# Kernel tuning notes

Measured on AMD Instinct MI355X. Metric: run time of the kernel, lower is better.

Reference implementation:

```python
import jax, jax.numpy as jnp
import numpy as np

N = 50000
E = 800000
IN_C = 128
HID = 64
OUT_C = 64
NUM_CLASSES = 10
H1 = 2
H2 = 1
NEG_SLOPE = 0.2  # PyG GATv2Conv default


def setup_inputs() -> dict:
    key = jax.random.key(0)
    ks = jax.random.split(key, 12)
    s = 0.05
    inp = {
        "x": jax.random.normal(ks[0], (N, IN_C), jnp.float32),
        "edge_index": jax.random.randint(ks[1], (2, E), 0, N, jnp.int64),
        "batch": jnp.zeros((N,), jnp.int64),
        # conv1 params (GATv2: separate lin_l / lin_r, att vector, output bias)
        "Wl1": jax.random.normal(ks[2], (H1 * HID, IN_C), jnp.float32) * s,
        "bl1": jnp.zeros((H1 * HID,), jnp.float32),
        "Wr1": jax.random.normal(ks[3], (H1 * HID, IN_C), jnp.float32) * s,
        "br1": jnp.zeros((H1 * HID,), jnp.float32),
        "att1": jax.random.normal(ks[4], (H1, HID), jnp.float32) * s,
        "bias1": jnp.zeros((H1 * HID,), jnp.float32),
        # conv2 params
        "Wl2": jax.random.normal(ks[5], (H2 * OUT_C, H1 * HID), jnp.float32) * s,
        "bl2": jnp.zeros((H2 * OUT_C,), jnp.float32),
        "Wr2": jax.random.normal(ks[6], (H2 * OUT_C, H1 * HID), jnp.float32) * s,
        "br2": jnp.zeros((H2 * OUT_C,), jnp.float32),
        "att2": jax.random.normal(ks[7], (H2, OUT_C), jnp.float32) * s,
        "bias2": jnp.zeros((OUT_C,), jnp.float32),
        # classifier head
        "Wc": jax.random.normal(ks[8], (NUM_CLASSES, OUT_C), jnp.float32) * s,
        "bc": jnp.zeros((NUM_CLASSES,), jnp.float32),
    }
    return inp


def _gatv2_conv(x, src, dst, Wl, bl, Wr, br, att, bias, heads, ch, concat):
    n = x.shape[0]
    xl = (x @ Wl.T + bl).reshape(n, heads, ch)  # messages from source
    xr = (x @ Wr.T + br).reshape(n, heads, ch)  # target-side transform
    e = xl[src] + xr[dst]                        # [Etot, H, C]
    e = jnp.where(e > 0, e, NEG_SLOPE * e)       # LeakyReLU
    score = jnp.einsum('ehc,hc->eh', e, att)     # [Etot, H]
    # segment softmax over incoming edges of each dst node
    m = jax.ops.segment_max(score, dst, num_segments=n)  # [N, H]
    m = jnp.where(jnp.isfinite(m), m, 0.0)
    ex = jnp.exp(score - m[dst])
    denom = jax.ops.segment_sum(ex, dst, num_segments=n)  # [N, H]
    alpha = ex / denom[dst]
    out = jax.ops.segment_sum(alpha[:, :, None] * xl[src], dst, num_segments=n)  # [N,H,C]
    if concat:
        out = out.reshape(n, heads * ch)
    else:
        out = out.mean(axis=1)
    return out + bias


def reference(x, edge_index, batch, Wl1, bl1, Wr1, br1, att1, bias1,
              Wl2, bl2, Wr2, br2, att2, bias2, Wc, bc):
    n = x.shape[0]
    # PyG GATv2Conv adds self-loops by default
    loops = jnp.arange(n, dtype=edge_index.dtype)
    src = jnp.concatenate([edge_index[0], loops])
    dst = jnp.concatenate([edge_index[1], loops])

    h = _gatv2_conv(x, src, dst, Wl1, bl1, Wr1, br1, att1, bias1, H1, HID, True)
    h = jax.nn.elu(h)  # dropout p=0 / eval -> identity
    h = _gatv2_conv(h, src, dst, Wl2, bl2, Wr2, br2, att2, bias2, H2, OUT_C, False)
    h = jax.nn.elu(h)
    logits = h @ Wc.T + bc  # [N, num_classes]
    return logits
```

## Files before the change

kernel.cpp:

```cpp
#include <hip/hip_runtime.h>
#include <hip/hip_bf16.h>

#define N_NODES 50000
#define E_EDGES 800000
#define NCLS 10
#define SCAN_BLOCKS 196

typedef short bfrag __attribute__((ext_vector_type(8)));
typedef float f32x4 __attribute__((ext_vector_type(4)));

__device__ __forceinline__ int rfl(int v) { return __builtin_amdgcn_readfirstlane(v); }

__device__ __forceinline__ unsigned short bf16rne(float x) {
    unsigned u = __float_as_uint(x);
    unsigned r = u + 0x7FFFu + ((u >> 16) & 1u);
    return (unsigned short)(r >> 16);
}

template <int CTRL, int RM>
__device__ __forceinline__ float dppadd(float x) {
    int s = __builtin_amdgcn_update_dpp(0, __float_as_int(x), CTRL, RM, 0xf, true);
    return x + __int_as_float(s);
}
__device__ __forceinline__ float rl63(float x) {
    return __int_as_float(__builtin_amdgcn_readlane(__float_as_int(x), 63));
}
__device__ __forceinline__ float rl31(float x) {
    return __int_as_float(__builtin_amdgcn_readlane(__float_as_int(x), 31));
}
__device__ __forceinline__ void dred1(float& x0) {
    x0 = dppadd<0x111, 0xf>(x0);
    x0 = dppadd<0x112, 0xf>(x0);
    x0 = dppadd<0x114, 0xf>(x0);
    x0 = dppadd<0x118, 0xf>(x0);
    x0 = dppadd<0x142, 0xa>(x0);
    x0 = dppadd<0x143, 0xc>(x0);
}
__device__ __forceinline__ void dred4(float& x0, float& x1, float& x2, float& x3) {
    x0 = dppadd<0x111, 0xf>(x0); x1 = dppadd<0x111, 0xf>(x1);
    x2 = dppadd<0x111, 0xf>(x2); x3 = dppadd<0x111, 0xf>(x3);
    x0 = dppadd<0x112, 0xf>(x0); x1 = dppadd<0x112, 0xf>(x1);
    x2 = dppadd<0x112, 0xf>(x2); x3 = dppadd<0x112, 0xf>(x3);
    x0 = dppadd<0x114, 0xf>(x0); x1 = dppadd<0x114, 0xf>(x1);
    x2 = dppadd<0x114, 0xf>(x2); x3 = dppadd<0x114, 0xf>(x3);
    x0 = dppadd<0x118, 0xf>(x0); x1 = dppadd<0x118, 0xf>(x1);
    x2 = dppadd<0x118, 0xf>(x2); x3 = dppadd<0x118, 0xf>(x3);
    x0 = dppadd<0x142, 0xa>(x0); x1 = dppadd<0x142, 0xa>(x1);
    x2 = dppadd<0x142, 0xa>(x2); x3 = dppadd<0x142, 0xa>(x3);
    x0 = dppadd<0x143, 0xc>(x0); x1 = dppadd<0x143, 0xc>(x1);
    x2 = dppadd<0x143, 0xc>(x2); x3 = dppadd<0x143, 0xc>(x3);
}
__device__ __forceinline__ void dredH(float& x) {
    x = dppadd<0x111, 0xf>(x);
    x = dppadd<0x112, 0xf>(x);
    x = dppadd<0x114, 0xf>(x);
    x = dppadd<0x118, 0xf>(x);
    x = dppadd<0x142, 0xa>(x);
}
__device__ __forceinline__ void dredH2(float& x, float& y) {
    x = dppadd<0x111, 0xf>(x); y = dppadd<0x111, 0xf>(y);
    x = dppadd<0x112, 0xf>(x); y = dppadd<0x112, 0xf>(y);
    x = dppadd<0x114, 0xf>(x); y = dppadd<0x114, 0xf>(y);
    x = dppadd<0x118, 0xf>(x); y = dppadd<0x118, 0xf>(y);
    x = dppadd<0x142, 0xa>(x); y = dppadd<0x142, 0xa>(y);
}
__device__ __forceinline__ float lrelu(float u) { return u > 0.f ? u : 0.2f * u; }
__device__ __forceinline__ float escore(float2 v, float2 xr2, float2 av) {
    float ux = v.x + xr2.x, uy = v.y + xr2.y;
    ux = fmaxf(ux, 0.2f * ux);
    uy = fmaxf(uy, 0.2f * uy);
    return ux * av.x + uy * av.y;
}

__global__ void k_count(const int* __restrict__ dst, int* __restrict__ deg) {
    int i = blockIdx.x * blockDim.x + threadIdx.x;
    if (i < E_EDGES) {
        unsigned d = (unsigned)dst[i];
        if (d < N_NODES) atomicAdd(&deg[d], 1);
    }
}

__global__ void k_scanA(const int* __restrict__ deg, int* __restrict__ incl,
                        int* __restrict__ bsum) {
    __shared__ int s[256];
    int i = blockIdx.x * 256 + threadIdx.x;
    int v = (i < N_NODES) ? deg[i] : 0;
    s[threadIdx.x] = v;
    __syncthreads();
    for (int off = 1; off < 256; off <<= 1) {
        int t = (threadIdx.x >= off) ? s[threadIdx.x - off] : 0;
        __syncthreads();
        s[threadIdx.x] += t;
        __syncthreads();
    }
    if (i < N_NODES) incl[i] = s[threadIdx.x];
    if (threadIdx.x == 255) bsum[blockIdx.x] = s[255];
}

__global__ void k_scanB(int* __restrict__ bsum) {
    __shared__ int s[256];
    int t = threadIdx.x;
    s[t] = (t < SCAN_BLOCKS) ? bsum[t] : 0;
    __syncthreads();
    for (int off = 1; off < 256; off <<= 1) {
        int v = (t >= off) ? s[t - off] : 0;
        __syncthreads();
        s[t] += v;
        __syncthreads();
    }
    if (t < SCAN_BLOCKS) bsum[t] = s[t];
}

__global__ void k_scanC(int* __restrict__ degcur, const int* __restrict__ incl,
                        const int* __restrict__ bsum, int* __restrict__ rowptr) {
    int i = blockIdx.x * 256 + threadIdx.x;
    if (i >= N_NODES) return;
    int base = (blockIdx.x == 0) ? 0 : bsum[blockIdx.x - 1];
    int d = degcur[i];
    int excl = base + incl[i] - d;
    rowptr[i] = excl;
    degcur[i] = excl;
    if (i == N_NODES - 1) rowptr[N_NODES] = base + incl[i];
}

__global__ void k_scatter(const int* __restrict__ src, const int* __restrict__ dst,
                          int* __restrict__ cursor, int* __restrict__ csr_src) {
    int i = blockIdx.x * blockDim.x + threadIdx.x;
    if (i < E_EDGES) {
        unsigned d = (unsigned)dst[i];
        if (d < N_NODES) {
            int p = atomicAdd(&cursor[d], 1);
            unsigned s = (unsigned)src[i];
            csr_src[p] = (s < N_NODES) ? (int)s : 0;
        }
    }
}

__global__ void k_splitW2(const float* __restrict__ WL, const float* __restrict__ WR,
                          int n, short* __restrict__ hiL, short* __restrict__ loL,
                          short* __restrict__ hiR, short* __restrict__ loR) {
    int i = blockIdx.x * 256 + threadIdx.x;
    if (i < n) {
        float x = WL[i];
        unsigned short h = bf16rne(x);
        float hf = __uint_as_float((unsigned)h << 16);
        hiL[i] = (short)h;
        loL[i] = (short)bf16rne(x - hf);
        float y = WR[i];
        unsigned short h2 = bf16rne(y);
        float hf2 = __uint_as_float((unsigned)h2 << 16);
        hiR[i] = (short)h2;
        loR[i] = (short)bf16rne(y - hf2);
    }
}

template <int NOUT>
__global__ __launch_bounds__(256) void k_mgemmS(const float* __restrict__ X,
                                                const short* __restrict__ whiL,
                                                const short* __restrict__ wloL,
                                                const short* __restrict__ whiR,
                                                const short* __restrict__ wloR,
                                                const float* __restrict__ bL,
                                                const float* __restrict__ bR,
                                                float* __restrict__ YL,
                                                float* __restrict__ YR, int nrows) {
    const int NCT = 4;
    const short* whi = blockIdx.z ? whiR : whiL;
    const short* wlo = blockIdx.z ? wloR : wloL;
    const float* b   = blockIdx.z ? bR : bL;
    float* Y         = blockIdx.z ? YR : YL;
    int tid = threadIdx.x;
    int wv = tid >> 6, lane = tid & 63;
    int m = lane & 15, g = lane >> 4;
    int colbase = blockIdx.y * 64;
    int row = blockIdx.x * 64 + wv * 16 + m;
    int rowc = min(row, nrows - 1);

    bfrag ahi[4], alo[4];
    const float* xp = X + (size_t)rowc * 128 + g * 8;
#pragma unroll
    for (int kb = 0; kb < 4; ++kb) {
        float4 u0 = *(const float4*)(xp + kb * 32);
        float4 u1 = *(const float4*)(xp + kb * 32 + 4);
        float xs[8] = {u0.x, u0.y, u0.z, u0.w, u1.x, u1.y, u1.z, u1.w};
#pragma unroll
        for (int j = 0; j < 8; ++j) {
            unsigned short h = bf16rne(xs[j]);
            float hf = __uint_as_float((unsigned)h << 16);
            unsigned short l = bf16rne(xs[j] - hf);
            ahi[kb][j] = (short)h;
            alo[kb][j] = (short)l;
        }
    }

    f32x4 acc[NCT];
#pragma unroll
    for (int ct = 0; ct < NCT; ++ct) acc[ct] = (f32x4){0.f, 0.f, 0.f, 0.f};

#pragma unroll
    for (int kb = 0; kb < 4; ++kb) {
#pragma unroll
        for (int ct = 0; ct < NCT; ++ct) {
            size_t wo = (size_t)(colbase + ct * 16 + m) * 128 + kb * 32 + g * 8;
            bfrag bh = *(const bfrag*)(whi + wo);
            bfrag bl_ = *(const bfrag*)(wlo + wo);
            acc[ct] = __builtin_amdgcn_mfma_f32_16x16x32_bf16(ahi[kb], bh, acc[ct], 0, 0, 0);
            acc[ct] = __builtin_amdgcn_mfma_f32_16x16x32_bf16(alo[kb], bh, acc[ct], 0, 0, 0);
            acc[ct] = __builtin_amdgcn_mfma_f32_16x16x32_bf16(ahi[kb], bl_, acc[ct], 0, 0, 0);
        }
    }

    int orow0 = blockIdx.x * 64 + wv * 16 + g * 4;
#pragma unroll
    for (int ct = 0; ct < NCT; ++ct) {
        int col = colbase + ct * 16 + m;
        float bv = b[col];
#pragma unroll
        for (int i = 0; i < 4; ++i) {
            int orow = orow0 + i;
            if (orow < nrows) Y[(size_t)orow * NOUT + col] = acc[ct][i] + bv;
        }
    }
}

__global__ __launch_bounds__(256) void k_gat1(const float* __restrict__ xl,
                                              const float* __restrict__ xr,
                                              const int* __restrict__ rowptr,
                                              const int* __restrict__ csr,
                                              const float* __restrict__ att,
                                              const float* __restrict__ bias,
                                              float* __restrict__ out) {
    int node = blockIdx.x * 4 + (threadIdx.x >> 6);
    if (node >= N_NODES) return;
    node = rfl(node);
    int lane = threadIdx.x & 63;
    bool lo = lane < 32;
    const float2* xl2 = (const float2*)xl;
    size_t nb = (size_t)node * 64;
    float2 av = ((const float2*)att)[lane];
    float2 xr2 = ((const float2*)xr)[nb + lane];
    float2 sl2 = xl2[nb + lane];

    float p = escore(sl2, xr2, av);
    dredH(p);
    float sv = lo ? rl31(p) : rl63(p);
    float ev = __expf(sv);
    float den = ev;
    float2 acc;
    acc.x = ev * sl2.x;
    acc.y = ev * sl2.y;

    int beg = rfl(rowptr[node]), end = rfl(rowptr[node + 1]);
    int cnt = end - beg;
    int np = cnt >> 1;
    if (np > 0) {
        const int* cp = csr + beg;
        int i0 = rfl(cp[0]), i1 = rfl(cp[1]);
        float2 A = xl2[(size_t)(unsigned)i0 * 64 + lane];
        float2 B = xl2[(size_t)(unsigned)i1 * 64 + lane];
        for (int q = 1; q <= np; ++q) {
            float2 nA = {0.f, 0.f}, nB = {0.f, 0.f};
            if (q < np) {
                int j0 = rfl(cp[2 * q]), j1 = rfl(cp[2 * q + 1]);
                nA = xl2[(size_t)(unsigned)j0 * 64 + lane];
                nB = xl2[(size_t)(unsigned)j1 * 64 + lane];
            }
            float pa = escore(A, xr2, av);
            float pb = escore(B, xr2, av);
            dredH2(pa, pb);
            float sa = lo ? rl31(pa) : rl63(pa);
            float sb = lo ? rl31(pb) : rl63(pb);
            float eva = __expf(sa);
            float evb = __expf(sb);
            den += eva + evb;
            acc.x = fmaf(eva, A.x, fmaf(evb, B.x, acc.x));
            acc.y = fmaf(eva, A.y, fmaf(evb, B.y, acc.y));
            A = nA; B = nB;
        }
    }
    if (cnt & 1) {
        int j = rfl(csr[end - 1]);
        float2 C = xl2[(size_t)(unsigned)j * 64 + lane];
        float pc = escore(C, xr2, av);
        dredH(pc);
        float sc = lo ? rl31(pc) : rl63(pc);
        float evc = __expf(sc);
        den += evc;
        acc.x = fmaf(evc, C.x, acc.x);
        acc.y = fmaf(evc, C.y, acc.y);
    }
    float2 b2 = ((const float2*)bias)[lane];
    float ox = acc.x / den + b2.x;
    float oy = acc.y / den + b2.y;
    ox = ox > 0.f ? ox : expm1f(ox);
    oy = oy > 0.f ? oy : expm1f(oy);
    float2 o2 = {ox, oy};
    ((float2*)out)[nb + lane] = o2;
}

__global__ __launch_bounds__(256) void k_gat2(const float* __restrict__ xl,
                                              const float* __restrict__ xr,
                                              const int* __restrict__ rowptr,
                                              const int* __restrict__ csr,
                                              const float* __restrict__ att,
                                              const float* __restrict__ bias,
                                              float* __restrict__ out) {
    int node = blockIdx.x * 4 + (threadIdx.x >> 6);
    if (node >= N_NODES) return;
    node = rfl(node);
    int lane = threadIdx.x & 63;
    float a = att[lane];
    size_t nb = (size_t)node << 6;
    float xrv = xr[nb + lane];
    float slv = xl[nb + lane];
    float p = lrelu(slv + xrv) * a;
    dred1(p);
    float w = __expf(rl63(p));
    float den = w;
    float acc = w * slv;

    int beg = rfl(rowptr[node]), end = rfl(rowptr[node + 1]);
    int cnt = end - beg;
    int quads = cnt >> 2;
    if (quads > 0) {
        const int* cp = csr + beg;
        int i0 = rfl(cp[0]), i1 = rfl(cp[1]), i2 = rfl(cp[2]), i3 = rfl(cp[3]);
        float A = (xl + ((size_t)(unsigned)i0 << 6))[lane];
        float B = (xl + ((size_t)(unsigned)i1 << 6))[lane];
        float C = (xl + ((size_t)(unsigned)i2 << 6))[lane];
        float D = (xl + ((size_t)(unsigned)i3 << 6))[lane];
        for (int q = 1; q <= quads; ++q) {
            float nA = 0.f, nB = 0.f, nC = 0.f, nD = 0.f;
            if (q < quads) {
                int j0 = rfl(cp[4 * q]), j1 = rfl(cp[4 * q + 1]);
                int j2 = rfl(cp[4 * q + 2]), j3 = rfl(cp[4 * q + 3]);
                nA = (xl + ((size_t)(unsigned)j0 << 6))[lane];
                nB = (xl + ((size_t)(unsigned)j1 << 6))[lane];
                nC = (xl + ((size_t)(unsigned)j2 << 6))[lane];
                nD = (xl + ((size_t)(unsigned)j3 << 6))[lane];
            }
            float pa = lrelu(A + xrv) * a;
            float pb = lrelu(B + xrv) * a;
            float pc = lrelu(C + xrv) * a;
            float pd = lrelu(D + xrv) * a;
            dred4(pa, pb, pc, pd);
            float ea = __expf(rl63(pa)), eb = __expf(rl63(pb));
            float ec = __expf(rl63(pc)), ed = __expf(rl63(pd));
            den += (ea + eb) + (ec + ed);
            acc = fmaf(ea, A, fmaf(eb, B, fmaf(ec, C, fmaf(ed, D, acc))));
            A = nA; B = nB; C = nC; D = nD;
        }
    }
    int rem = cnt & 3;
    if (rem) {
        int j0 = rfl(csr[end - rem]);
        int j1 = (rem > 1) ? rfl(csr[end - rem + 1]) : j0;
        int j2 = (rem > 2) ? rfl(csr[end - rem + 2]) : j0;
        float A = (xl + ((size_t)(unsigned)j0 << 6))[lane];
        float B = (xl + ((size_t)(unsigned)j1 << 6))[lane];
        float C = (xl + ((size_t)(unsigned)j2 << 6))[lane];
        float pa = lrelu(A + xrv) * a;
        float pb = lrelu(B + xrv) * a;
        float pc = lrelu(C + xrv) * a;
        float pd = 0.f;
        dred4(pa, pb, pc, pd);
        float ea = __expf(rl63(pa));
        float eb = (rem > 1) ? __expf(rl63(pb)) : 0.f;
        float ec = (rem > 2) ? __expf(rl63(pc)) : 0.f;
        den += ea + eb + ec;
        acc = fmaf(ea, A, fmaf(eb, B, fmaf(ec, C, acc)));
    }
    float o = acc / den + bias[lane];
    out[nb + lane] = o > 0.f ? o : expm1f(o);
}

__global__ __launch_bounds__(256) void k_head(const float* __restrict__ H,
                                              const float* __restrict__ Wc,
                                              const float* __restrict__ bc,
                                              float* __restrict__ out) {
    __shared__ float Ws[NCLS * 64];
    __shared__ float bs[NCLS];
    for (int i = threadIdx.x; i < NCLS * 64; i += 256) Ws[i] = Wc[i];
    if (threadIdx.x < NCLS) bs[threadIdx.x] = bc[threadIdx.x];
    __syncthreads();
    int n = blockIdx.x * 256 + threadIdx.x;
    if (n >= N_NODES) return;
    const float4* hp = (const float4*)(H + (size_t)n * 64);
    float acc[NCLS] = {};
#pragma unroll
    for (int k4 = 0; k4 < 16; ++k4) {
        float4 hv = hp[k4];
#pragma unroll
        for (int c = 0; c < NCLS; ++c) {
            acc[c] = fmaf(hv.x, Ws[c * 64 + k4 * 4 + 0], acc[c]);
            acc[c] = fmaf(hv.y, Ws[c * 64 + k4 * 4 + 1], acc[c]);
            acc[c] = fmaf(hv.z, Ws[c * 64 + k4 * 4 + 2], acc[c]);
            acc[c] = fmaf(hv.w, Ws[c * 64 + k4 * 4 + 3], acc[c]);
        }
    }
#pragma unroll
    for (int c = 0; c < NCLS; ++c) out[(size_t)n * NCLS + c] = acc[c] + bs[c];
}

extern "C" void kernel_launch(void* const* d_in, const int* in_sizes, int n_in,
                              void* d_out, int out_size, void* d_ws, size_t ws_size,
                              hipStream_t stream) {
    const float* x     = (const float*)d_in[0];
    const int*   ei    = (const int*)d_in[1];
    const int*   srcp  = ei;
    const int*   dstp  = ei + E_EDGES;
    const float* Wl1   = (const float*)d_in[3];
    const float* bl1   = (const float*)d_in[4];
    const float* Wr1   = (const float*)d_in[5];
    const float* br1   = (const float*)d_in[6];
    const float* att1  = (const float*)d_in[7];
    const float* bias1 = (const float*)d_in[8];
    const float* Wl2   = (const float*)d_in[9];
    const float* bl2   = (const float*)d_in[10];
    const float* Wr2   = (const float*)d_in[11];
    const float* br2   = (const float*)d_in[12];
    const float* att2  = (const float*)d_in[13];
    const float* bias2 = (const float*)d_in[14];
    const float* Wc    = (const float*)d_in[15];
    const float* bc    = (const float*)d_in[16];

    float* fA = (float*)d_ws;
    float* fB = fA + (size_t)N_NODES * 128;
    float* fC = fB + (size_t)N_NODES * 128;
    int* rowptr = (int*)(fC + (size_t)N_NODES * 128);
    int* degcur = rowptr + (N_NODES + 1);
    int* csr    = degcur + N_NODES;
    size_t woff = ((size_t)(csr + E_EDGES) - (size_t)d_ws + 15) & ~(size_t)15;
    short* whiL = (short*)((char*)d_ws + woff);
    short* wloL = whiL + 16384;
    short* whiR = wloL + 16384;
    short* wloR = whiR + 16384;
    int* incl = (int*)(wloR + 16384);
    int* bsum = incl + N_NODES;

    hipMemsetAsync(degcur, 0, N_NODES * sizeof(int), stream);
    k_count<<<(E_EDGES + 255) / 256, 256, 0, stream>>>(dstp, degcur);
    k_scanA<<<SCAN_BLOCKS, 256, 0, stream>>>(degcur, incl, bsum);
    k_scanB<<<1, 256, 0, stream>>>(bsum);
    k_scanC<<<SCAN_BLOCKS, 256, 0, stream>>>(degcur, incl, bsum, rowptr);
    k_scatter<<<(E_EDGES + 255) / 256, 256, 0, stream>>>(srcp, dstp, degcur, csr);

    int gblocks = (N_NODES + 63) / 64;

    k_splitW2<<<64, 256, 0, stream>>>(Wl1, Wr1, 16384, whiL, wloL, whiR, wloR);
    dim3 g1(gblocks, 2, 2);
    k_mgemmS<128><<<g1, 256, 0, stream>>>(x, whiL, wloL, whiR, wloR, bl1, br1, fA, fB, N_NODES);
    k_gat1<<<(N_NODES + 3) / 4, 256, 0, stream>>>(fA, fB, rowptr, csr, att1, bias1, fC);

    k_splitW2<<<32, 256, 0, stream>>>(Wl2, Wr2, 8192, whiL, wloL, whiR, wloR);
    dim3 g2(gblocks, 1, 2);
    k_mgemmS<64><<<g2, 256, 0, stream>>>(fC, whiL, wloL, whiR, wloR, bl2, br2, fA, fB, N_NODES);
    k_gat2<<<(N_NODES + 3) / 4, 256, 0, stream>>>(fA, fB, rowptr, csr, att2, bias2, fC);

    k_head<<<(N_NODES + 255) / 256, 256, 0, stream>>>(fC, Wc, bc, (float*)d_out);
}
```

Baseline: 412.9 us.

## Stage weight tiles in LDS and process multiple row tiles per GEMM block

The split-bf16 GEMM kernel now copies its 64-column hi/lo weight slice into padded shared memory once per block, then loops over four 64-row tiles, reading B fragments from LDS instead of global memory. The grid shrinks by the same factor, so weights are loaded and reused across more rows. The risks are lower parallelism for the GEMMs, with fewer blocks and a serial loop over row tiles, and about 34KB of LDS per block limiting occupancy.

```diff
diff --git a/kernel.cpp b/kernel.cpp
--- a/kernel.cpp
+++ b/kernel.cpp
@@ -154,7 +154,7 @@
     }
 }
 
-template <int NOUT>
+template <int NOUT, int RT>
 __global__ __launch_bounds__(256) void k_mgemmS(const float* __restrict__ X,
                                                 const short* __restrict__ whiL,
                                                 const short* __restrict__ wloL,
@@ -165,60 +165,78 @@
                                                 float* __restrict__ YL,
                                                 float* __restrict__ YR, int nrows) {
     const int NCT = 4;
+    const int KP = 136;
+    __shared__ short Bhi[64 * KP];
+    __shared__ short Blo[64 * KP];
     const short* whi = blockIdx.z ? whiR : whiL;
     const short* wlo = blockIdx.z ? wloR : wloL;
     const float* b   = blockIdx.z ? bR : bL;
     float* Y         = blockIdx.z ? YR : YL;
     int tid = threadIdx.x;
+    int colbase = blockIdx.y * 64;
+
+    for (int idx = tid; idx < 64 * 16; idx += 256) {
+        int col = idx >> 4;
+        int k8 = (idx & 15) * 8;
+        size_t srco = (size_t)(colbase + col) * 128 + k8;
+        *(int4*)&Bhi[col * KP + k8] = *(const int4*)&whi[srco];
+        *(int4*)&Blo[col * KP + k8] = *(const int4*)&wlo[srco];
+    }
+    __syncthreads();
+
     int wv = tid >> 6, lane = tid & 63;
     int m = lane & 15, g = lane >> 4;
-    int colbase = blockIdx.y * 64;
-    int row = blockIdx.x * 64 + wv * 16 + m;
-    int rowc = min(row, nrows - 1);
-
-    bfrag ahi[4], alo[4];
-    const float* xp = X + (size_t)rowc * 128 + g * 8;
-#pragma unroll
-    for (int kb = 0; kb < 4; ++kb) {
-        float4 u0 = *(const float4*)(xp + kb * 32);
-        float4 u1 = *(const float4*)(xp + kb * 32 + 4);
-        float xs[8] = {u0.x, u0.y, u0.z, u0.w, u1.x, u1.y, u1.z, u1.w};
-#pragma unroll
-        for (int j = 0; j < 8; ++j) {
-            unsigned short h = bf16rne(xs[j]);
-            float hf = __uint_as_float((unsigned)h << 16);
-            unsigned short l = bf16rne(xs[j] - hf);
-            ahi[kb][j] = (short)h;
-            alo[kb][j] = (short)l;
-        }
-    }
-
-    f32x4 acc[NCT];
-#pragma unroll
-    for (int ct = 0; ct < NCT; ++ct) acc[ct] = (f32x4){0.f, 0.f, 0.f, 0.f};
-
-#pragma unroll
-    for (int kb = 0; kb < 4; ++kb) {
+
+    for (int rt = 0; rt < RT; ++rt) {
+        int rti = blockIdx.x * RT + rt;
+        if (rti * 64 >= nrows) break;
+        int row = rti * 64 + wv * 16 + m;
+        int rowc = min(row, nrows - 1);
+
+        bfrag ahi[4], alo[4];
+        const float* xp = X + (size_t)rowc * 128 + g * 8;
+#pragma unroll
+        for (int kb = 0; kb < 4; ++kb) {
+            float4 u0 = *(const float4*)(xp + kb * 32);
+            float4 u1 = *(const float4*)(xp + kb * 32 + 4);
+            float xs[8] = {u0.x, u0.y, u0.z, u0.w, u1.x, u1.y, u1.z, u1.w};
+#pragma unroll
+            for (int j = 0; j < 8; ++j) {
+                unsigned short h = bf16rne(xs[j]);
+                float hf = __uint_as_float((unsigned)h << 16);
+                unsigned short l = bf16rne(xs[j] - hf);
+                ahi[kb][j] = (short)h;
+                alo[kb][j] = (short)l;
+            }
+        }
+
+        f32x4 acc[NCT];
+#pragma unroll
+        for (int ct = 0; ct < NCT; ++ct) acc[ct] = (f32x4){0.f, 0.f, 0.f, 0.f};
+
+#pragma unroll
+        for (int kb = 0; kb < 4; ++kb) {
+#pragma unroll
+            for (int ct = 0; ct < NCT; ++ct) {
+                int lo_ = (ct * 16 + m) * KP + kb * 32 + g * 8;
+                bfrag bh = *(const bfrag*)&Bhi[lo_];
+                bfrag bl_ = *(const bfrag*)&Blo[lo_];
+                acc[ct] = __builtin_amdgcn_mfma_f32_16x16x32_bf16(ahi[kb], bh, acc[ct], 0, 0, 0);
+                acc[ct] = __builtin_amdgcn_mfma_f32_16x16x32_bf16(alo[kb], bh, acc[ct], 0, 0, 0);
+                acc[ct] = __builtin_amdgcn_mfma_f32_16x16x32_bf16(ahi[kb], bl_, acc[ct], 0, 0, 0);
+            }
+        }
+
+        int orow0 = rti * 64 + wv * 16 + g * 4;
 #pragma unroll
         for (int ct = 0; ct < NCT; ++ct) {
-            size_t wo = (size_t)(colbase + ct * 16 + m) * 128 + kb * 32 + g * 8;
-            bfrag bh = *(const bfrag*)(whi + wo);
-            bfrag bl_ = *(const bfrag*)(wlo + wo);
-            acc[ct] = __builtin_amdgcn_mfma_f32_16x16x32_bf16(ahi[kb], bh, acc[ct], 0, 0, 0);
-            acc[ct] = __builtin_amdgcn_mfma_f32_16x16x32_bf16(alo[kb], bh, acc[ct], 0, 0, 0);
-            acc[ct] = __builtin_amdgcn_mfma_f32_16x16x32_bf16(ahi[kb], bl_, acc[ct], 0, 0, 0);
-        }
-    }
-
-    int orow0 = blockIdx.x * 64 + wv * 16 + g * 4;
-#pragma unroll
-    for (int ct = 0; ct < NCT; ++ct) {
-        int col = colbase + ct * 16 + m;
-        float bv = b[col];
-#pragma unroll
-        for (int i = 0; i < 4; ++i) {
-            int orow = orow0 + i;
-            if (orow < nrows) Y[(size_t)orow * NOUT + col] = acc[ct][i] + bv;
+            int col = colbase + ct * 16 + m;
+            float bv = b[col];
+#pragma unroll
+            for (int i = 0; i < 4; ++i) {
+                int orow = orow0 + i;
+                if (orow < nrows) Y[(size_t)orow * NOUT + col] = acc[ct][i] + bv;
+            }
         }
     }
 }
@@ -445,16 +463,17 @@
     k_scanC<<<SCAN_BLOCKS, 256, 0, stream>>>(degcur, incl, bsum, rowptr);
     k_scatter<<<(E_EDGES + 255) / 256, 256, 0, stream>>>(srcp, dstp, degcur, csr);
 
-    int gblocks = (N_NODES + 63) / 64;
+    const int RT = 4;
+    int gx = (N_NODES + 64 * RT - 1) / (64 * RT);
 
     k_splitW2<<<64, 256, 0, stream>>>(Wl1, Wr1, 16384, whiL, wloL, whiR, wloR);
-    dim3 g1(gblocks, 2, 2);
-    k_mgemmS<128><<<g1, 256, 0, stream>>>(x, whiL, wloL, whiR, wloR, bl1, br1, fA, fB, N_NODES);
+    dim3 g1(gx, 2, 2);
+    k_mgemmS<128, RT><<<g1, 256, 0, stream>>>(x, whiL, wloL, whiR, wloR, bl1, br1, fA, fB, N_NODES);
     k_gat1<<<(N_NODES + 3) / 4, 256, 0, stream>>>(fA, fB, rowptr, csr, att1, bias1, fC);
 
     k_splitW2<<<32, 256, 0, stream>>>(Wl2, Wr2, 8192, whiL, wloL, whiR, wloR);
-    dim3 g2(gblocks, 1, 2);
-    k_mgemmS<64><<<g2, 256, 0, stream>>>(fC, whiL, wloL, whiR, wloR, bl2, br2, fA, fB, N_NODES);
+    dim3 g2(gx, 1, 2);
+    k_mgemmS<64, RT><<<g2, 256, 0, stream>>>(fC, whiL, wloL, whiR, wloR, bl2, br2, fA, fB, N_NODES);
     k_gat2<<<(N_NODES + 3) / 4, 256, 0, stream>>>(fA, fB, rowptr, csr, att2, bias2, fC);
 
     k_head<<<(N_NODES + 255) / 256, 256, 0, stream>>>(fC, Wc, bc, (float*)d_out);
```

After: 359.9 us. -12.8%, faster.
